# Optimization experiments

Measured on AMD Instinct MI355X. Metric: run time of the kernel, lower is better.

## Reference

```python
import jax, jax.numpy as jnp
import numpy as np

DIM = 1024
N_HEADS = 16
HEAD_DIM = DIM // N_HEADS


def setup_inputs() -> dict:
    key = jax.random.key(0)
    ks = jax.random.split(key, 6)
    s = DIM ** -0.5
    return {
        "x": jax.random.normal(ks[0], (2, 2048, DIM), dtype=jnp.float32),
        "Wq": jax.random.normal(ks[1], (DIM, DIM), dtype=jnp.float32) * s,
        "Wk": jax.random.normal(ks[2], (DIM, DIM), dtype=jnp.float32) * s,
        "Wv": jax.random.normal(ks[3], (DIM, DIM), dtype=jnp.float32) * s,
        "Wo": jax.random.normal(ks[4], (DIM, DIM), dtype=jnp.float32) * s,
        "bo": jax.random.normal(ks[5], (DIM,), dtype=jnp.float32) * 0.01,
    }


def reference(x, Wq, Wk, Wv, Wo, bo):
    B, T, C = x.shape
    H, D = N_HEADS, HEAD_DIM
    # Linear(dim, dim, bias=False): y = x @ W^T
    q = (x @ Wq.T).reshape(B, T, H, D).transpose(0, 2, 1, 3)  # B H T D
    k = (x @ Wk.T).reshape(B, T, H, D).transpose(0, 2, 1, 3)
    v = (x @ Wv.T).reshape(B, T, H, D).transpose(0, 2, 1, 3)
    q = q * (D ** -0.5)
    attn = jnp.einsum('bhqd,bhkd->bhqk', q, k)  # B H T T
    causal_mask = jnp.triu(jnp.ones((T, T), dtype=bool), k=1)
    attn = jnp.where(causal_mask, -jnp.inf, attn)
    attn = jax.nn.softmax(attn, axis=-1)
    out = jnp.einsum('bhqk,bhkd->bhqd', attn, v)  # B H T D
    out = out.transpose(0, 2, 1, 3).reshape(B, T, C)
    return out @ Wo.T + bo
```

## Files before the change

kernel.cpp:

```cpp
#include <hip/hip_runtime.h>
#include <math.h>

typedef __attribute__((ext_vector_type(8))) short bf16x8;
typedef __attribute__((ext_vector_type(4))) float f32x4;

__device__ __forceinline__ ushort f2bf(float f) {
  union { float f; unsigned u; } v; v.f = f;
  return (ushort)((v.u + 0x8000u) >> 16);
}

__device__ __forceinline__ void g2l16(const void* g, void* l) {
  __builtin_amdgcn_global_load_lds((const __attribute__((address_space(1))) unsigned*)g,
                                   (__attribute__((address_space(3))) unsigned*)l, 16, 0, 0);
}

__global__ __launch_bounds__(256) void cast_all(const float* __restrict__ x,
                                                const float* __restrict__ Wq,
                                                const float* __restrict__ Wk,
                                                const float* __restrict__ Wv,
                                                const float* __restrict__ Wo,
                                                ushort* __restrict__ xbf,
                                                ushort* __restrict__ wcat) {
  int i = blockIdx.x * 256 + threadIdx.x;
  if (i < 1048576) {
    float4 v = ((const float4*)x)[i];
    ushort4 u; u.x = f2bf(v.x); u.y = f2bf(v.y); u.z = f2bf(v.z); u.w = f2bf(v.w);
    ((ushort4*)xbf)[i] = u;
  } else {
    int j = i - 1048576;
    int sel = j >> 18;
    const float* src = (sel == 0) ? Wq : (sel == 1) ? Wk : (sel == 2) ? Wv : Wo;
    float scale = (sel == 0) ? 0.125f * 1.44269504088896f : 1.0f;
    float4 v = ((const float4*)src)[j & 0x3FFFF];
    ushort4 u;
    u.x = f2bf(v.x * scale); u.y = f2bf(v.y * scale);
    u.z = f2bf(v.z * scale); u.w = f2bf(v.w * scale);
    ((ushort4*)wcat)[j] = u;
  }
}

__global__ __launch_bounds__(256) void gemm_qkv(const ushort* __restrict__ A,
                                                const ushort* __restrict__ B,
                                                ushort* __restrict__ QK,
                                                ushort* __restrict__ Vt) {
  const int K = 1024;
  __shared__ __align__(16) ushort As[2][128 * 32];
  __shared__ __align__(16) ushort Bs[2][128 * 32];
  const int m0 = blockIdx.y * 128, n0 = blockIdx.x * 128;
  const int tid = threadIdx.x, lane = tid & 63, wid = tid >> 6;
  const int quad = lane >> 4, lc = lane & 15;
  const int lrow = lane >> 2, lcol = (lane & 3) * 8;
  const int wm = (wid >> 1) * 64, wn = (wid & 1) * 64;

  f32x4 acc[4][4] = {};

  auto stage = [&](int k0, int nb) {
    const ushort* Ag = A + (size_t)(m0 + wid * 32 + lrow) * K + k0 + lcol;
    g2l16(Ag, &As[nb][wid * 1024]);
    g2l16(Ag + (size_t)16 * K, &As[nb][wid * 1024 + 512]);
    const ushort* Bg = B + (size_t)(n0 + wid * 32 + lrow) * K + k0 + lcol;
    g2l16(Bg, &Bs[nb][wid * 1024]);
    g2l16(Bg + (size_t)16 * K, &Bs[nb][wid * 1024 + 512]);
  };

  stage(0, 0);
  for (int k0 = 0; k0 < K; k0 += 32) {
    const int nb = (k0 >> 5) & 1;
    __syncthreads();
    if (k0 + 32 < K) stage(k0 + 32, nb ^ 1);

    bf16x8 af[4], bfr[4];
#pragma unroll
    for (int t = 0; t < 4; t++)
      af[t] = *(const bf16x8*)&As[nb][(wm + t * 16 + lc) * 32 + quad * 8];
#pragma unroll
    for (int t = 0; t < 4; t++)
      bfr[t] = *(const bf16x8*)&Bs[nb][(wn + t * 16 + lc) * 32 + quad * 8];
#pragma unroll
    for (int mt = 0; mt < 4; mt++)
#pragma unroll
      for (int nt = 0; nt < 4; nt++)
        acc[mt][nt] = __builtin_amdgcn_mfma_f32_16x16x32_bf16(af[mt], bfr[nt], acc[mt][nt], 0, 0, 0);
  }

  const int sel = n0 >> 10;
#pragma unroll
  for (int mt = 0; mt < 4; mt++) {
#pragma unroll
    for (int r = 0; r < 4; r++) {
      int row = m0 + wm + mt * 16 + quad * 4 + r;
#pragma unroll
      for (int nt = 0; nt < 4; nt++) {
        int col = n0 + wn + nt * 16 + lc;
        ushort v = f2bf(acc[mt][nt][r]);
        if (sel < 2) {
          QK[((size_t)sel << 22) + (size_t)row * 1024 + (col & 1023)] = v;
        } else {
          int hd = col & 1023;
          size_t bh = (size_t)((row >> 11) * 16 + (hd >> 6));
          Vt[bh * 131072 + (size_t)(hd & 63) * 2048 + (row & 2047)] = v;
        }
      }
    }
  }
}

__global__ __launch_bounds__(256) void gemm_proj(const ushort* __restrict__ A,
                                                 const ushort* __restrict__ B,
                                                 float* __restrict__ C,
                                                 const float* __restrict__ bias) {
  const int K = 1024;
  __shared__ __align__(16) ushort As[2][2][128 * 32];
  __shared__ __align__(16) ushort Bs[2][2][64 * 32];
  const int m0 = blockIdx.y * 128, n0 = blockIdx.x * 64;
  const int tid = threadIdx.x, lane = tid & 63, wid = tid >> 6;
  const int quad = lane >> 4, lc = lane & 15;
  const int lrow = lane >> 2, lcol = (lane & 3) * 8;
  const int wm = (wid >> 1) * 64, wn = (wid & 1) * 32;

  f32x4 acc[4][2] = {};

  auto stage = [&](int k0, int nb) {
    const ushort* Ag = A + (size_t)(m0 + wid * 32 + lrow) * K + k0 + lcol;
    g2l16(Ag,                      &As[nb][0][wid * 1024]);
    g2l16(Ag + (size_t)16 * K,     &As[nb][0][wid * 1024 + 512]);
    g2l16(Ag + 32,                 &As[nb][1][wid * 1024]);
    g2l16(Ag + (size_t)16 * K + 32, &As[nb][1][wid * 1024 + 512]);
    const ushort* Bg = B + (size_t)(n0 + wid * 16 + lrow) * K + k0 + lcol;
    g2l16(Bg,      &Bs[nb][0][wid * 512]);
    g2l16(Bg + 32, &Bs[nb][1][wid * 512]);
  };

  stage(0, 0);
  for (int k0 = 0; k0 < K; k0 += 64) {
    const int nb = (k0 >> 6) & 1;
    __syncthreads();
    if (k0 + 64 < K) stage(k0 + 64, nb ^ 1);

#pragma unroll
    for (int ks = 0; ks < 2; ks++) {
      bf16x8 af[4], bfr[2];
#pragma unroll
      for (int t = 0; t < 4; t++)
        af[t] = *(const bf16x8*)&As[nb][ks][(wm + t * 16 + lc) * 32 + quad * 8];
#pragma unroll
      for (int t = 0; t < 2; t++)
        bfr[t] = *(const bf16x8*)&Bs[nb][ks][(wn + t * 16 + lc) * 32 + quad * 8];
#pragma unroll
      for (int mt = 0; mt < 4; mt++)
#pragma unroll
        for (int nt = 0; nt < 2; nt++)
          acc[mt][nt] = __builtin_amdgcn_mfma_f32_16x16x32_bf16(af[mt], bfr[nt], acc[mt][nt], 0, 0, 0);
    }
  }

#pragma unroll
  for (int mt = 0; mt < 4; mt++) {
#pragma unroll
    for (int r = 0; r < 4; r++) {
      int row = m0 + wm + mt * 16 + quad * 4 + r;
#pragma unroll
      for (int nt = 0; nt < 2; nt++) {
        int col = n0 + wn + nt * 16 + lc;
        C[(size_t)row * 1024 + col] = acc[mt][nt][r] + bias[col];
      }
    }
  }
}

__global__ __launch_bounds__(256, 6) void attn_kernel(const ushort* __restrict__ Qb,
                                                      const ushort* __restrict__ Kb,
                                                      const ushort* __restrict__ Vt,
                                                      float* __restrict__ O32,
                                                      float* __restrict__ L32) {
  __shared__ __align__(16) ushort Ks[2][64 * 32];
  __shared__ __align__(16) ushort Vs[2][64 * 32];
  __shared__ __align__(16) ushort Ps[4][16][72];

  const int bh = blockIdx.y, b = bh >> 4, h = bh & 15;
  const int f = 79 - (int)blockIdx.x;
  int qi, ci;
  if (f < 8)       { qi = f;                 ci = 0; }
  else if (f < 24) { int g = f - 8;  qi = 8  + (g >> 1); ci = g & 1; }
  else if (f < 48) { int g = f - 24; int q3 = g / 3; qi = 16 + q3; ci = g - 3 * q3; }
  else             { int g = f - 48; qi = 24 + (g >> 2); ci = g & 3; }

  const int t0 = ci * 8;
  const int t1 = min(t0 + 8, qi + 1);
  const int qb_block = qi * 64;

  const int tid = threadIdx.x, lane = tid & 63, wid = tid >> 6;
  const int quad = lane >> 4, lc = lane & 15;
  const int lrow = lane >> 2, lcol = (lane & 3) * 8;
  const int qbw = qb_block + wid * 16;

  const size_t kbase = (size_t)(b * 2048) * 1024 + h * 64;
  const size_t vbase = (size_t)bh * 131072;

  const ushort* Qp = Qb + kbase + (size_t)(qbw + lc) * 1024;
  bf16x8 qf0 = *(const bf16x8*)(Qp + quad * 8);
  bf16x8 qf1 = *(const bf16x8*)(Qp + 32 + quad * 8);

  f32x4 o_acc[4] = {};
  float l_r[4] = {0.f, 0.f, 0.f, 0.f};

  for (int kt = t0; kt < t1; kt++) {
    const int kb = kt * 64;
    __syncthreads();
#pragma unroll
    for (int cc = 0; cc < 2; cc++) {
      int ck = wid + cc * 4;
      int half = ck >> 2, rg = ck & 3;
      const ushort* gK = Kb + kbase + (size_t)(kb + rg * 16 + lrow) * 1024 + half * 32 + lcol;
      g2l16(gK, &Ks[half][rg * 512]);
      const ushort* gV = Vt + vbase + (size_t)(rg * 16 + lrow) * 2048 + kb + half * 32 + lcol;
      g2l16(gV, &Vs[half][rg * 512]);
    }
    __syncthreads();

    const bool diag = (kb + 63 > qbw);
#pragma unroll
    for (int c = 0; c < 4; c++) {
      bf16x8 kf0 = *(const bf16x8*)&Ks[0][(c * 16 + lc) * 32 + quad * 8];
      bf16x8 kf1 = *(const bf16x8*)&Ks[1][(c * 16 + lc) * 32 + quad * 8];
      f32x4 z = {};
      z = __builtin_amdgcn_mfma_f32_16x16x32_bf16(qf0, kf0, z, 0, 0, 0);
      z = __builtin_amdgcn_mfma_f32_16x16x32_bf16(qf1, kf1, z, 0, 0, 0);
#pragma unroll
      for (int r = 0; r < 4; r++) {
        float sv = z[r];
        if (diag && (kb + c * 16 + lc > qbw + quad * 4 + r)) sv = -1e30f;
        float pv = __builtin_amdgcn_exp2f(sv);
        l_r[r] += pv;
        Ps[wid][quad * 4 + r][c * 16 + lc] = f2bf(pv);
      }
    }
    __asm__ volatile("s_waitcnt lgkmcnt(0)" ::: "memory");
    bf16x8 ap0 = *(const bf16x8*)&Ps[wid][lc][quad * 8];
    bf16x8 ap1 = *(const bf16x8*)&Ps[wid][lc][32 + quad * 8];

#pragma unroll
    for (int nt = 0; nt < 4; nt++) {
      bf16x8 vb0 = *(const bf16x8*)&Vs[0][(nt * 16 + lc) * 32 + quad * 8];
      bf16x8 vb1 = *(const bf16x8*)&Vs[1][(nt * 16 + lc) * 32 + quad * 8];
      o_acc[nt] = __builtin_amdgcn_mfma_f32_16x16x32_bf16(ap0, vb0, o_acc[nt], 0, 0, 0);
      o_acc[nt] = __builtin_amdgcn_mfma_f32_16x16x32_bf16(ap1, vb1, o_acc[nt], 0, 0, 0);
    }
  }

#pragma unroll
  for (int r = 0; r < 4; r++) {
    float s_ = l_r[r];
    s_ += __shfl_xor(s_, 1);
    s_ += __shfl_xor(s_, 2);
    s_ += __shfl_xor(s_, 4);
    s_ += __shfl_xor(s_, 8);
    l_r[r] = s_;
  }
  if (lc == 0) {
#pragma unroll
    for (int r = 0; r < 4; r++)
      atomicAdd(&L32[(size_t)bh * 2048 + qbw + quad * 4 + r], l_r[r]);
  }
#pragma unroll
  for (int r = 0; r < 4; r++) {
    size_t orow = ((size_t)(b * 2048) + qbw + quad * 4 + r) * 1024 + h * 64 + lc;
#pragma unroll
    for (int nt = 0; nt < 4; nt++)
      atomicAdd(&O32[orow + nt * 16], o_acc[nt][r]);
  }
}

__global__ __launch_bounds__(256) void normalize_kernel(const float* __restrict__ O32,
                                                        const float* __restrict__ L32,
                                                        ushort* __restrict__ Out) {
  const int row = blockIdx.x;
  const int tid = threadIdx.x;
  const int col = tid * 4;
  const int b = row >> 11, t = row & 2047, h = col >> 6;
  const float inv = 1.0f / L32[(size_t)(b * 16 + h) * 2048 + t];
  float4 o = ((const float4*)(O32 + (size_t)row * 1024))[tid];
  ushort4 u;
  u.x = f2bf(o.x * inv); u.y = f2bf(o.y * inv);
  u.z = f2bf(o.z * inv); u.w = f2bf(o.w * inv);
  ((ushort4*)(Out + (size_t)row * 1024))[tid] = u;
}

extern "C" void kernel_launch(void* const* d_in, const int* in_sizes, int n_in,
                              void* d_out, int out_size, void* d_ws, size_t ws_size,
                              hipStream_t stream) {
  const float* x  = (const float*)d_in[0];
  const float* Wq = (const float*)d_in[1];
  const float* Wk = (const float*)d_in[2];
  const float* Wv = (const float*)d_in[3];
  const float* Wo = (const float*)d_in[4];
  const float* bo = (const float*)d_in[5];
  float* out = (float*)d_out;

  char* ws = (char*)d_ws;
  ushort* xbf  = (ushort*)(ws);
  ushort* wcat = (ushort*)(ws + (8ull  << 20));
  ushort* qkv  = (ushort*)(ws + (16ull << 20));
  ushort* Qp   = qkv;
  ushort* Kp   = qkv + (1ull << 22);
  ushort* Vt   = qkv + (2ull << 22);
  float*  L32  = (float*)ws;
  float*  O32  = out;
  ushort* attn_out = Qp;

  cast_all<<<8192, 256, 0, stream>>>(x, Wq, Wk, Wv, Wo, xbf, wcat);

  gemm_qkv<<<dim3(24, 32), 256, 0, stream>>>(xbf, wcat, qkv, Vt);

  hipMemsetAsync(L32, 0, (size_t)32 * 2048 * 4, stream);
  hipMemsetAsync(O32, 0, (size_t)4096 * 1024 * 4, stream);

  attn_kernel<<<dim3(80, 32), 256, 0, stream>>>(Qp, Kp, Vt, O32, L32);

  normalize_kernel<<<4096, 256, 0, stream>>>(O32, L32, attn_out);

  gemm_proj<<<dim3(16, 32), 256, 0, stream>>>(
      attn_out, wcat + (size_t)3072 * 1024, out, bo);
}
```

Baseline: 215.9 us.

## Double attention query tile per wave, split V transpose, fuse output zeroing

The attention kernel now processes 32 query rows per wave (128 per block) instead of 16, reusing each staged K/V tile across two query sub-tiles, which halves the grid and retunes the split schedule. The QKV GEMM epilogue writes V row-major with coalesced stores, and a separate tile-based kernel transposes V. Zeroing of the O32 accumulator moves into the cast kernel, replacing a memset. The change adds register pressure (occupancy hint drops from 6 to 4) and an extra launch plus a pass over V in exchange for fewer K/V reloads and cheaper GEMM stores.

```diff
diff --git a/kernel.cpp b/kernel.cpp
--- a/kernel.cpp
+++ b/kernel.cpp
@@ -20,13 +20,14 @@
                                                 const float* __restrict__ Wv,
                                                 const float* __restrict__ Wo,
                                                 ushort* __restrict__ xbf,
-                                                ushort* __restrict__ wcat) {
+                                                ushort* __restrict__ wcat,
+                                                float4* __restrict__ O32) {
   int i = blockIdx.x * 256 + threadIdx.x;
   if (i < 1048576) {
     float4 v = ((const float4*)x)[i];
     ushort4 u; u.x = f2bf(v.x); u.y = f2bf(v.y); u.z = f2bf(v.z); u.w = f2bf(v.w);
     ((ushort4*)xbf)[i] = u;
-  } else {
+  } else if (i < 2097152) {
     int j = i - 1048576;
     int sel = j >> 18;
     const float* src = (sel == 0) ? Wq : (sel == 1) ? Wk : (sel == 2) ? Wv : Wo;
@@ -36,13 +37,14 @@
     u.x = f2bf(v.x * scale); u.y = f2bf(v.y * scale);
     u.z = f2bf(v.z * scale); u.w = f2bf(v.w * scale);
     ((ushort4*)wcat)[j] = u;
+  } else {
+    O32[i - 2097152] = float4{0.f, 0.f, 0.f, 0.f};
   }
 }
 
 __global__ __launch_bounds__(256) void gemm_qkv(const ushort* __restrict__ A,
                                                 const ushort* __restrict__ B,
-                                                ushort* __restrict__ QK,
-                                                ushort* __restrict__ Vt) {
+                                                ushort* __restrict__ C3) {
   const int K = 1024;
   __shared__ __align__(16) ushort As[2][128 * 32];
   __shared__ __align__(16) ushort Bs[2][128 * 32];
@@ -83,7 +85,6 @@
         acc[mt][nt] = __builtin_amdgcn_mfma_f32_16x16x32_bf16(af[mt], bfr[nt], acc[mt][nt], 0, 0, 0);
   }
 
-  const int sel = n0 >> 10;
 #pragma unroll
   for (int mt = 0; mt < 4; mt++) {
 #pragma unroll
@@ -92,14 +93,8 @@
 #pragma unroll
       for (int nt = 0; nt < 4; nt++) {
         int col = n0 + wn + nt * 16 + lc;
-        ushort v = f2bf(acc[mt][nt][r]);
-        if (sel < 2) {
-          QK[((size_t)sel << 22) + (size_t)row * 1024 + (col & 1023)] = v;
-        } else {
-          int hd = col & 1023;
-          size_t bh = (size_t)((row >> 11) * 16 + (hd >> 6));
-          Vt[bh * 131072 + (size_t)(hd & 63) * 2048 + (row & 2047)] = v;
-        }
+        size_t dst = ((size_t)(col >> 10) << 22) + (size_t)row * 1024 + (col & 1023);
+        C3[dst] = f2bf(acc[mt][nt][r]);
       }
     }
   }
@@ -122,9 +117,9 @@
 
   auto stage = [&](int k0, int nb) {
     const ushort* Ag = A + (size_t)(m0 + wid * 32 + lrow) * K + k0 + lcol;
-    g2l16(Ag,                      &As[nb][0][wid * 1024]);
-    g2l16(Ag + (size_t)16 * K,     &As[nb][0][wid * 1024 + 512]);
-    g2l16(Ag + 32,                 &As[nb][1][wid * 1024]);
+    g2l16(Ag,                       &As[nb][0][wid * 1024]);
+    g2l16(Ag + (size_t)16 * K,      &As[nb][0][wid * 1024 + 512]);
+    g2l16(Ag + 32,                  &As[nb][1][wid * 1024]);
     g2l16(Ag + (size_t)16 * K + 32, &As[nb][1][wid * 1024 + 512]);
     const ushort* Bg = B + (size_t)(n0 + wid * 16 + lrow) * K + k0 + lcol;
     g2l16(Bg,      &Bs[nb][0][wid * 512]);
@@ -168,41 +163,70 @@
   }
 }
 
-__global__ __launch_bounds__(256, 6) void attn_kernel(const ushort* __restrict__ Qb,
+__global__ __launch_bounds__(256) void transpose_v(const ushort* __restrict__ Vb,
+                                                   ushort* __restrict__ Vt) {
+  __shared__ ushort tile[64][72];
+  const int bh = blockIdx.y, b = bh >> 4, h = bh & 15;
+  const int tt = blockIdx.x;
+  const int tid = threadIdx.x;
+#pragma unroll
+  for (int i = 0; i < 2; i++) {
+    int idx = i * 256 + tid;
+    int trow = idx >> 3;
+    int dcol = (idx & 7) * 8;
+    uint4 v = *(const uint4*)(Vb + (size_t)(b * 2048 + tt * 64 + trow) * 1024 + h * 64 + dcol);
+    ushort e[8]; *(uint4*)e = v;
+#pragma unroll
+    for (int j = 0; j < 8; j++) tile[dcol + j][trow] = e[j];
+  }
+  __syncthreads();
+#pragma unroll
+  for (int i = 0; i < 2; i++) {
+    int idx = i * 256 + tid;
+    int drow = idx >> 3;
+    int tloc = (idx & 7) * 8;
+    uint4 v = *(const uint4*)&tile[drow][tloc];
+    *(uint4*)(Vt + (size_t)bh * 131072 + (size_t)drow * 2048 + tt * 64 + tloc) = v;
+  }
+}
+
+__global__ __launch_bounds__(256, 4) void attn_kernel(const ushort* __restrict__ Qb,
                                                       const ushort* __restrict__ Kb,
                                                       const ushort* __restrict__ Vt,
                                                       float* __restrict__ O32,
                                                       float* __restrict__ L32) {
   __shared__ __align__(16) ushort Ks[2][64 * 32];
   __shared__ __align__(16) ushort Vs[2][64 * 32];
-  __shared__ __align__(16) ushort Ps[4][16][72];
+  __shared__ __align__(16) ushort Ps[4][32][72];
 
   const int bh = blockIdx.y, b = bh >> 4, h = bh & 15;
-  const int f = 79 - (int)blockIdx.x;
+  const int f = (int)blockIdx.x;
   int qi, ci;
-  if (f < 8)       { qi = f;                 ci = 0; }
-  else if (f < 24) { int g = f - 8;  qi = 8  + (g >> 1); ci = g & 1; }
-  else if (f < 48) { int g = f - 24; int q3 = g / 3; qi = 16 + q3; ci = g - 3 * q3; }
-  else             { int g = f - 48; qi = 24 + (g >> 2); ci = g & 3; }
-
+  if (f < 16)      { qi = 12 + (f >> 2); ci = f & 3; }
+  else if (f < 28) { int g = f - 16; int q3 = g / 3; qi = 8 + q3; ci = g - 3 * q3; }
+  else if (f < 36) { int g = f - 28; qi = 4 + (g >> 1); ci = g & 1; }
+  else             { qi = f - 36; ci = 0; }
   const int t0 = ci * 8;
-  const int t1 = min(t0 + 8, qi + 1);
-  const int qb_block = qi * 64;
+  const int t1 = min(t0 + 8, 2 * qi + 2);
 
   const int tid = threadIdx.x, lane = tid & 63, wid = tid >> 6;
   const int quad = lane >> 4, lc = lane & 15;
   const int lrow = lane >> 2, lcol = (lane & 3) * 8;
-  const int qbw = qb_block + wid * 16;
+  const int qbw = qi * 128 + wid * 32;
 
   const size_t kbase = (size_t)(b * 2048) * 1024 + h * 64;
   const size_t vbase = (size_t)bh * 131072;
 
-  const ushort* Qp = Qb + kbase + (size_t)(qbw + lc) * 1024;
-  bf16x8 qf0 = *(const bf16x8*)(Qp + quad * 8);
-  bf16x8 qf1 = *(const bf16x8*)(Qp + 32 + quad * 8);
-
-  f32x4 o_acc[4] = {};
-  float l_r[4] = {0.f, 0.f, 0.f, 0.f};
+  bf16x8 qf[2][2];
+#pragma unroll
+  for (int t = 0; t < 2; t++) {
+    const ushort* Qp = Qb + kbase + (size_t)(qbw + t * 16 + lc) * 1024;
+    qf[t][0] = *(const bf16x8*)(Qp + quad * 8);
+    qf[t][1] = *(const bf16x8*)(Qp + 32 + quad * 8);
+  }
+
+  f32x4 o_acc[2][4] = {};
+  float l_r[2][4] = {};
 
   for (int kt = t0; kt < t1; kt++) {
     const int kb = kt * 64;
@@ -218,56 +242,69 @@
     }
     __syncthreads();
 
-    const bool diag = (kb + 63 > qbw);
 #pragma unroll
     for (int c = 0; c < 4; c++) {
       bf16x8 kf0 = *(const bf16x8*)&Ks[0][(c * 16 + lc) * 32 + quad * 8];
       bf16x8 kf1 = *(const bf16x8*)&Ks[1][(c * 16 + lc) * 32 + quad * 8];
-      f32x4 z = {};
-      z = __builtin_amdgcn_mfma_f32_16x16x32_bf16(qf0, kf0, z, 0, 0, 0);
-      z = __builtin_amdgcn_mfma_f32_16x16x32_bf16(qf1, kf1, z, 0, 0, 0);
-#pragma unroll
-      for (int r = 0; r < 4; r++) {
-        float sv = z[r];
-        if (diag && (kb + c * 16 + lc > qbw + quad * 4 + r)) sv = -1e30f;
-        float pv = __builtin_amdgcn_exp2f(sv);
-        l_r[r] += pv;
-        Ps[wid][quad * 4 + r][c * 16 + lc] = f2bf(pv);
+#pragma unroll
+      for (int t = 0; t < 2; t++) {
+        f32x4 z = {};
+        z = __builtin_amdgcn_mfma_f32_16x16x32_bf16(qf[t][0], kf0, z, 0, 0, 0);
+        z = __builtin_amdgcn_mfma_f32_16x16x32_bf16(qf[t][1], kf1, z, 0, 0, 0);
+        const bool diag = (kb + 63 > qbw + t * 16);
+#pragma unroll
+        for (int r = 0; r < 4; r++) {
+          float sv = z[r];
+          if (diag && (kb + c * 16 + lc > qbw + t * 16 + quad * 4 + r)) sv = -1e30f;
+          float pv = __builtin_amdgcn_exp2f(sv);
+          l_r[t][r] += pv;
+          Ps[wid][t * 16 + quad * 4 + r][c * 16 + lc] = f2bf(pv);
+        }
       }
     }
     __asm__ volatile("s_waitcnt lgkmcnt(0)" ::: "memory");
-    bf16x8 ap0 = *(const bf16x8*)&Ps[wid][lc][quad * 8];
-    bf16x8 ap1 = *(const bf16x8*)&Ps[wid][lc][32 + quad * 8];
+    bf16x8 ap[2][2];
+#pragma unroll
+    for (int t = 0; t < 2; t++) {
+      ap[t][0] = *(const bf16x8*)&Ps[wid][t * 16 + lc][quad * 8];
+      ap[t][1] = *(const bf16x8*)&Ps[wid][t * 16 + lc][32 + quad * 8];
+    }
 
 #pragma unroll
     for (int nt = 0; nt < 4; nt++) {
       bf16x8 vb0 = *(const bf16x8*)&Vs[0][(nt * 16 + lc) * 32 + quad * 8];
       bf16x8 vb1 = *(const bf16x8*)&Vs[1][(nt * 16 + lc) * 32 + quad * 8];
-      o_acc[nt] = __builtin_amdgcn_mfma_f32_16x16x32_bf16(ap0, vb0, o_acc[nt], 0, 0, 0);
-      o_acc[nt] = __builtin_amdgcn_mfma_f32_16x16x32_bf16(ap1, vb1, o_acc[nt], 0, 0, 0);
-    }
-  }
-
-#pragma unroll
-  for (int r = 0; r < 4; r++) {
-    float s_ = l_r[r];
-    s_ += __shfl_xor(s_, 1);
-    s_ += __shfl_xor(s_, 2);
-    s_ += __shfl_xor(s_, 4);
-    s_ += __shfl_xor(s_, 8);
-    l_r[r] = s_;
-  }
-  if (lc == 0) {
-#pragma unroll
-    for (int r = 0; r < 4; r++)
-      atomicAdd(&L32[(size_t)bh * 2048 + qbw + quad * 4 + r], l_r[r]);
-  }
-#pragma unroll
-  for (int r = 0; r < 4; r++) {
-    size_t orow = ((size_t)(b * 2048) + qbw + quad * 4 + r) * 1024 + h * 64 + lc;
-#pragma unroll
-    for (int nt = 0; nt < 4; nt++)
-      atomicAdd(&O32[orow + nt * 16], o_acc[nt][r]);
+#pragma unroll
+      for (int t = 0; t < 2; t++) {
+        o_acc[t][nt] = __builtin_amdgcn_mfma_f32_16x16x32_bf16(ap[t][0], vb0, o_acc[t][nt], 0, 0, 0);
+        o_acc[t][nt] = __builtin_amdgcn_mfma_f32_16x16x32_bf16(ap[t][1], vb1, o_acc[t][nt], 0, 0, 0);
+      }
+    }
+  }
+
+#pragma unroll
+  for (int t = 0; t < 2; t++) {
+#pragma unroll
+    for (int r = 0; r < 4; r++) {
+      float s_ = l_r[t][r];
+      s_ += __shfl_xor(s_, 1);
+      s_ += __shfl_xor(s_, 2);
+      s_ += __shfl_xor(s_, 4);
+      s_ += __shfl_xor(s_, 8);
+      l_r[t][r] = s_;
+    }
+    if (lc == 0) {
+#pragma unroll
+      for (int r = 0; r < 4; r++)
+        atomicAdd(&L32[(size_t)bh * 2048 + qbw + t * 16 + quad * 4 + r], l_r[t][r]);
+    }
+#pragma unroll
+    for (int r = 0; r < 4; r++) {
+      size_t orow = ((size_t)(b * 2048) + qbw + t * 16 + quad * 4 + r) * 1024 + h * 64 + lc;
+#pragma unroll
+      for (int nt = 0; nt < 4; nt++)
+        atomicAdd(&O32[orow + nt * 16], o_acc[t][nt][r]);
+    }
   }
 }
 
@@ -303,19 +340,21 @@
   ushort* qkv  = (ushort*)(ws + (16ull << 20));
   ushort* Qp   = qkv;
   ushort* Kp   = qkv + (1ull << 22);
-  ushort* Vt   = qkv + (2ull << 22);
-  float*  L32  = (float*)ws;
+  ushort* Vp   = qkv + (2ull << 22);
+  ushort* Vt   = (ushort*)(ws);
+  float*  L32  = (float*)Vp;
   float*  O32  = out;
   ushort* attn_out = Qp;
 
-  cast_all<<<8192, 256, 0, stream>>>(x, Wq, Wk, Wv, Wo, xbf, wcat);
-
-  gemm_qkv<<<dim3(24, 32), 256, 0, stream>>>(xbf, wcat, qkv, Vt);
+  cast_all<<<12288, 256, 0, stream>>>(x, Wq, Wk, Wv, Wo, xbf, wcat, (float4*)O32);
+
+  gemm_qkv<<<dim3(24, 32), 256, 0, stream>>>(xbf, wcat, qkv);
+
+  transpose_v<<<dim3(32, 32), 256, 0, stream>>>(Vp, Vt);
 
   hipMemsetAsync(L32, 0, (size_t)32 * 2048 * 4, stream);
-  hipMemsetAsync(O32, 0, (size_t)4096 * 1024 * 4, stream);
-
-  attn_kernel<<<dim3(80, 32), 256, 0, stream>>>(Qp, Kp, Vt, O32, L32);
+
+  attn_kernel<<<dim3(40, 32), 256, 0, stream>>>(Qp, Kp, Vt, O32, L32);
 
   normalize_kernel<<<4096, 256, 0, stream>>>(O32, L32, attn_out);
 
```

Result: no change. 212.5 us (-1.6%).
